# Kernel tuning notes

Measured on AMD Instinct MI355X. Metric: run time of the kernel, lower is better.

The kernel has to match this reference:

```python
import jax, jax.numpy as jnp
import numpy as np

B, T, C, H = 4, 4096, 1024, 64

def setup_inputs() -> dict:
    key = jax.random.key(0)
    k1, k2, k3, k4 = jax.random.split(key, 4)
    x = jax.random.normal(k1, (B, T, C), dtype=jnp.float32)
    # nn.Linear(C, H, bias=False): y = x @ W^T with W [H, C]; store as [C, H] for x @ W
    Wq = jax.random.normal(k2, (C, H), dtype=jnp.float32) * (C ** -0.5)
    Wk = jax.random.normal(k3, (C, H), dtype=jnp.float32) * (C ** -0.5)
    Wv = jax.random.normal(k4, (C, H), dtype=jnp.float32) * (C ** -0.5)
    return {"x": x, "Wq": Wq, "Wk": Wk, "Wv": Wv}

def reference(x, Wq, Wk, Wv):
    # Manual causal single-head attention (dropout p=0 -> identity).
    q = x @ Wq  # [B, T, H]
    k = x @ Wk  # [B, T, H]
    v = x @ Wv  # [B, T, H]
    scale = q.shape[-1] ** -0.5
    w = jnp.einsum('bth,bsh->bts', q, k) * scale  # [B, T, T] scores
    causal = jnp.tril(jnp.ones((x.shape[1], x.shape[1]), dtype=bool))
    w = jnp.where(causal, w, -jnp.inf)
    w = jax.nn.softmax(w, axis=-1)
    out = jnp.einsum('bts,bsh->bth', w, v)  # [B, T, H]
    return out
```

## Files before the change

kernel.cpp:

```cpp
#include <hip/hip_runtime.h>
#include <math.h>

#define Bn 4
#define Tn 4096
#define Cn 1024
#define Hn 64

typedef __attribute__((ext_vector_type(8))) short short8;
typedef __attribute__((ext_vector_type(4))) float floatx4;
typedef unsigned short ushort_t;

#define QSCALE 0.1803368801111204f

__device__ __forceinline__ ushort_t f2bf(float f) {
  union { float f; unsigned u; } v; v.f = f;
  unsigned r = v.u + 0x7FFFu + ((v.u >> 16) & 1u);
  return (ushort_t)(r >> 16);
}
__device__ __forceinline__ ushort_t f2bf_hu(float f) {
  union { float f; unsigned u; } v; v.f = f;
  return (ushort_t)((v.u + 0x8000u) >> 16);
}
__device__ __forceinline__ float bf2f(ushort_t h) {
  union { unsigned u; float f; } v; v.u = ((unsigned)h) << 16; return v.f;
}


__global__ __launch_bounds__(256) void wf_kernel(
    const float* __restrict__ Wq, const float* __restrict__ Wk,
    const float* __restrict__ Wv, ushort_t* __restrict__ Wf)
{
  __shared__ float ws[32][65];
  const int tid = threadIdx.x;
  const int m = blockIdx.x >> 5;
  const int g = blockIdx.x & 31;
  const float* W = (m == 0) ? Wq : (m == 1) ? Wk : Wv;
  const float4* src = (const float4*)(W + (size_t)g * 32 * Hn);
#pragma unroll
  for (int it = 0; it < 2; ++it) {
    int i4 = it * 256 + tid;
    float4 v = src[i4];
    int c = i4 >> 4, h = (i4 & 15) * 4;
    ws[c][h] = v.x; ws[c][h + 1] = v.y; ws[c][h + 2] = v.z; ws[c][h + 3] = v.w;
  }
  __syncthreads();
  const int nt = tid >> 6, lane = tid & 63;
  const int col = lane & 15, quad = lane >> 4;
  ushort_t t[8];
#pragma unroll
  for (int e = 0; e < 8; ++e) t[e] = f2bf(ws[quad * 8 + e][nt * 16 + col]);
  *(short8*)(Wf + ((size_t)((m * 32 + g) * 4 + nt) * 64 + lane) * 8) = *(short8*)t;
}

__global__ __launch_bounds__(256, 2) void qkv_proj_kernel(
    const float* __restrict__ x, const ushort_t* __restrict__ Wf,
    ushort_t* __restrict__ Qf, ushort_t* __restrict__ Kf,
    ushort_t* __restrict__ Vf)
{
  __shared__ __align__(16) char smem[49152];
  ushort_t* red = (ushort_t*)smem;
  ushort_t* img = (ushort_t*)smem;

  const int tid  = threadIdx.x;
  const int wv   = tid >> 6;
  const int lane = tid & 63;
  const int col  = lane & 15;
  const int quad = lane >> 4;
  const int blk  = blockIdx.x;
  const int row0 = blk * 32;

  floatx4 acc[2][3][4];
#pragma unroll
  for (int sub = 0; sub < 2; ++sub)
#pragma unroll
    for (int m = 0; m < 3; ++m)
#pragma unroll
      for (int nt = 0; nt < 4; ++nt) {
        acc[sub][m][nt][0] = 0.f; acc[sub][m][nt][1] = 0.f;
        acc[sub][m][nt][2] = 0.f; acc[sub][m][nt][3] = 0.f;
      }

#pragma unroll
  for (int ch = 0; ch < 8; ++ch) {
    const int gg = wv * 8 + ch;
    short8 af[2];
#pragma unroll
    for (int sub = 0; sub < 2; ++sub) {
      const float* xp = x + (size_t)(row0 + sub * 16 + col) * Cn + gg * 32 + quad * 8;
      float4 a0 = *(const float4*)(xp);
      float4 a1 = *(const float4*)(xp + 4);
      ushort_t t[8];
      t[0] = f2bf(a0.x); t[1] = f2bf(a0.y); t[2] = f2bf(a0.z); t[3] = f2bf(a0.w);
      t[4] = f2bf(a1.x); t[5] = f2bf(a1.y); t[6] = f2bf(a1.z); t[7] = f2bf(a1.w);
      af[sub] = *(short8*)t;
    }
#pragma unroll
    for (int m = 0; m < 3; ++m)
#pragma unroll
      for (int nt = 0; nt < 4; ++nt) {
        short8 bf = *(const short8*)(Wf + ((size_t)((m * 32 + gg) * 4 + nt) * 64 + lane) * 8);
        acc[0][m][nt] = __builtin_amdgcn_mfma_f32_16x16x32_bf16(af[0], bf, acc[0][m][nt], 0, 0, 0);
        acc[1][m][nt] = __builtin_amdgcn_mfma_f32_16x16x32_bf16(af[1], bf, acc[1][m][nt], 0, 0, 0);
      }
  }

#pragma unroll
  for (int sub = 0; sub < 2; ++sub)
#pragma unroll
    for (int m = 0; m < 3; ++m)
#pragma unroll
      for (int nt = 0; nt < 4; ++nt) {
        const int p = (sub * 3 + m) * 4 + nt;
        ushort4 u;
        u.x = f2bf(acc[sub][m][nt][0]); u.y = f2bf(acc[sub][m][nt][1]);
        u.z = f2bf(acc[sub][m][nt][2]); u.w = f2bf(acc[sub][m][nt][3]);
        *(ushort4*)&red[((p * 4 + wv) * 64 + lane) * 4] = u;
      }
  __syncthreads();

  float v[6][4];
#pragma unroll
  for (int pp = 0; pp < 6; ++pp) {
    const int p = wv * 6 + pp;
    ushort4 w0 = *(const ushort4*)&red[((p * 4 + 0) * 64 + lane) * 4];
    ushort4 w1 = *(const ushort4*)&red[((p * 4 + 1) * 64 + lane) * 4];
    ushort4 w2 = *(const ushort4*)&red[((p * 4 + 2) * 64 + lane) * 4];
    ushort4 w3 = *(const ushort4*)&red[((p * 4 + 3) * 64 + lane) * 4];
    v[pp][0] = (bf2f(w0.x) + bf2f(w1.x)) + (bf2f(w2.x) + bf2f(w3.x));
    v[pp][1] = (bf2f(w0.y) + bf2f(w1.y)) + (bf2f(w2.y) + bf2f(w3.y));
    v[pp][2] = (bf2f(w0.z) + bf2f(w1.z)) + (bf2f(w2.z) + bf2f(w3.z));
    v[pp][3] = (bf2f(w0.w) + bf2f(w1.w)) + (bf2f(w2.w) + bf2f(w3.w));
  }
  __syncthreads();

#pragma unroll
  for (int pp = 0; pp < 6; ++pp) {
    const int p = wv * 6 + pp;
    const int sub = (p >= 12) ? 1 : 0;
    const int mrem = p - sub * 12;
    const int m = mrem >> 2, nt = mrem & 3;
#pragma unroll
    for (int r = 0; r < 4; ++r) {
      const int tlq = quad * 4 + r;
      if (m == 2) {
        img[4096 + nt * 512 + (tlq >> 2) * 128 + col * 8 + (tlq & 3) * 2 + sub] = f2bf(v[pp][r]);
      } else {
        const int h = nt * 16 + col;
        const int idx = (h >> 5) * 512 + ((h >> 3) & 3) * 128 + tlq * 8 + (h & 7);
        img[m * 2048 + sub * 1024 + idx] = f2bf(m == 0 ? v[pp][r] * QSCALE : v[pp][r]);
      }
    }
  }
  __syncthreads();

  {
    const int b = blk >> 7, g = blk & 127;
#pragma unroll
    for (int sub = 0; sub < 2; ++sub) {
      const size_t qg = (size_t)(b * 256 + 2 * g + sub) * 1024 + tid * 4;
      *(uint2*)(Qf + qg) = *(const uint2*)&img[sub * 1024 + tid * 4];
      *(uint2*)(Kf + qg) = *(const uint2*)&img[2048 + sub * 1024 + tid * 4];
    }
    const int ht = tid >> 6;
    const size_t vg = ((size_t)(b * 64 + (g >> 1)) * 8 + ht * 2 + (g & 1)) * 512 + (tid & 63) * 8;
    *(short8*)(Vf + vg) = *(const short8*)&img[4096 + ht * 512 + (tid & 63) * 8];
  }
}

__global__ __launch_bounds__(256, 2) void attn_kernel(
    const ushort_t* __restrict__ Qf, const ushort_t* __restrict__ Kf,
    const ushort_t* __restrict__ Vf, float* __restrict__ out)
{
  __shared__ __align__(16) ushort_t Ps[4][2][16][72];
  __shared__ __align__(16) float Om[4][2][16][68];
  __shared__ __align__(16) float Ml[4][2][16];

  const int tid  = threadIdx.x;
  const int wv   = tid >> 6;
  const int lane = tid & 63;
  const int col  = lane & 15;
  const int quad = lane >> 4;
  const int b = blockIdx.x & 3;
  const int g = 127 - (blockIdx.x >> 2);

  short8 qf[2][2];
#pragma unroll
  for (int sub = 0; sub < 2; ++sub)
#pragma unroll
    for (int half = 0; half < 2; ++half)
      qf[sub][half] = *(const short8*)(Qf + (size_t)(b * 256 + 2 * g + sub) * 1024 + half * 512 + lane * 8);

  const ushort_t* Kbase = Kf + (size_t)b * 256 * 1024;
  const ushort_t* Vbase = Vf + (size_t)b * 64 * 8 * 512;

  short8 ones;
#pragma unroll
  for (int e = 0; e < 8; ++e) ones[e] = (short)0x3F80;

  floatx4 o[2][4], ol[2];
#pragma unroll
  for (int sub = 0; sub < 2; ++sub) {
#pragma unroll
    for (int ht = 0; ht < 4; ++ht) { o[sub][ht][0]=0.f; o[sub][ht][1]=0.f; o[sub][ht][2]=0.f; o[sub][ht][3]=0.f; }
    ol[sub][0]=0.f; ol[sub][1]=0.f; ol[sub][2]=0.f; ol[sub][3]=0.f;
  }

  const int ntile = ((g * 32 + 31) >> 6) + 1;
  const int dtile = ntile - 1;

  short8 kf[8], kfn[8];
#pragma unroll
  for (int kt = 0; kt < 4; ++kt) {
    const ushort_t* kp = Kbase + (size_t)wv * 4096 + kt * 1024 + lane * 8;
    kf[kt * 2]     = *(const short8*)(kp);
    kf[kt * 2 + 1] = *(const short8*)(kp + 512);
  }

  for (int i = wv; i < ntile; i += 4) {
    short8 vf[8];
#pragma unroll
    for (int ht = 0; ht < 4; ++ht) {
#pragma unroll
      for (int kh = 0; kh < 2; ++kh)
        vf[ht * 2 + kh] = *(const short8*)(Vbase + ((size_t)i * 8 + ht * 2 + kh) * 512 + lane * 8);
    }
#pragma unroll
    for (int kt = 0; kt < 4; ++kt) {
      const ushort_t* kp = Kbase + (size_t)(i + 4) * 4096 + kt * 1024 + lane * 8;
      kfn[kt * 2]     = *(const short8*)(kp);
      kfn[kt * 2 + 1] = *(const short8*)(kp + 512);
    }

    floatx4 s[2][4];
#pragma unroll
    for (int sub = 0; sub < 2; ++sub)
#pragma unroll
      for (int kt = 0; kt < 4; ++kt) {
        floatx4 c; c[0]=0.f; c[1]=0.f; c[2]=0.f; c[3]=0.f;
        c = __builtin_amdgcn_mfma_f32_16x16x32_bf16(qf[sub][0], kf[kt * 2],     c, 0, 0, 0);
        c = __builtin_amdgcn_mfma_f32_16x16x32_bf16(qf[sub][1], kf[kt * 2 + 1], c, 0, 0, 0);
        s[sub][kt] = c;
      }

    if (i == dtile) {
#pragma unroll
      for (int sub = 0; sub < 2; ++sub)
#pragma unroll
        for (int kt = 0; kt < 4; ++kt)
#pragma unroll
          for (int r = 0; r < 4; ++r)
            if (64 * i + kt * 16 + col > g * 32 + sub * 16 + quad * 4 + r)
              s[sub][kt][r] = -INFINITY;
    }

#pragma unroll
    for (int sub = 0; sub < 2; ++sub)
#pragma unroll
      for (int kt = 0; kt < 4; ++kt)
#pragma unroll
        for (int r = 0; r < 4; ++r)
          s[sub][kt][r] = __builtin_amdgcn_exp2f(s[sub][kt][r]);

#pragma unroll
    for (int sub = 0; sub < 2; ++sub)
#pragma unroll
      for (int r = 0; r < 4; ++r)
#pragma unroll
        for (int kh = 0; kh < 2; ++kh) {
          unsigned lo = f2bf_hu(s[sub][kh * 2][r]);
          unsigned hi = f2bf_hu(s[sub][kh * 2 + 1][r]);
          *(unsigned*)&Ps[wv][sub][quad * 4 + r][kh * 32 + col * 2] = (hi << 16) | lo;
        }

    short8 pf[2][2];
#pragma unroll
    for (int sub = 0; sub < 2; ++sub) {
      pf[sub][0] = *(const short8*)&Ps[wv][sub][col][quad * 8];
      pf[sub][1] = *(const short8*)&Ps[wv][sub][col][32 + quad * 8];
    }

#pragma unroll
    for (int sub = 0; sub < 2; ++sub) {
#pragma unroll
      for (int ht = 0; ht < 4; ++ht) {
        o[sub][ht] = __builtin_amdgcn_mfma_f32_16x16x32_bf16(pf[sub][0], vf[ht * 2],     o[sub][ht], 0, 0, 0);
        o[sub][ht] = __builtin_amdgcn_mfma_f32_16x16x32_bf16(pf[sub][1], vf[ht * 2 + 1], o[sub][ht], 0, 0, 0);
      }
      ol[sub] = __builtin_amdgcn_mfma_f32_16x16x32_bf16(pf[sub][0], ones, ol[sub], 0, 0, 0);
      ol[sub] = __builtin_amdgcn_mfma_f32_16x16x32_bf16(pf[sub][1], ones, ol[sub], 0, 0, 0);
    }

#pragma unroll
    for (int u2 = 0; u2 < 8; ++u2) kf[u2] = kfn[u2];
  }

#pragma unroll
  for (int sub = 0; sub < 2; ++sub) {
#pragma unroll
    for (int ht = 0; ht < 4; ++ht)
#pragma unroll
      for (int r = 0; r < 4; ++r)
        Om[wv][sub][quad * 4 + r][ht * 16 + col] = o[sub][ht][r];
    if (col == 0) {
#pragma unroll
      for (int r = 0; r < 4; ++r) Ml[wv][sub][quad * 4 + r] = ol[sub][r];
    }
  }
  __syncthreads();

  const int rr = tid >> 4, h4 = (tid & 15) * 4;
#pragma unroll
  for (int sub = 0; sub < 2; ++sub) {
    float L = (Ml[0][sub][rr] + Ml[1][sub][rr]) + (Ml[2][sub][rr] + Ml[3][sub][rr]);
    float4 a; a.x = 0.f; a.y = 0.f; a.z = 0.f; a.w = 0.f;
#pragma unroll
    for (int w = 0; w < 4; ++w) {
      float4 ov = *(const float4*)&Om[w][sub][rr][h4];
      a.x += ov.x; a.y += ov.y; a.z += ov.z; a.w += ov.w;
    }
    float inv = 1.f / L;
    a.x *= inv; a.y *= inv; a.z *= inv; a.w *= inv;
    *(float4*)(out + (size_t)(b * Tn + g * 32 + sub * 16 + rr) * Hn + h4) = a;
  }
}

extern "C" void kernel_launch(void* const* d_in, const int* in_sizes, int n_in,
                              void* d_out, int out_size, void* d_ws, size_t ws_size,
                              hipStream_t stream) {
  const float* x  = (const float*)d_in[0];
  const float* Wq = (const float*)d_in[1];
  const float* Wk = (const float*)d_in[2];
  const float* Wv = (const float*)d_in[3];
  float* out = (float*)d_out;

  ushort_t* Qf = (ushort_t*)d_ws;
  ushort_t* Kf = Qf + (size_t)Bn * Tn * Hn;
  ushort_t* Vf = Kf + (size_t)Bn * Tn * Hn;
  ushort_t* Wf = Vf + (size_t)Bn * Tn * Hn;

  wf_kernel<<<dim3(96), dim3(256), 0, stream>>>(Wq, Wk, Wv, Wf);
  qkv_proj_kernel<<<dim3(512), dim3(256), 0, stream>>>(x, Wf, Qf, Kf, Vf);
  attn_kernel<<<dim3(Bn * 128), dim3(256), 0, stream>>>(Qf, Kf, Vf, out);
}
```

Before: 134.2 us.

## Stage x tile through LDS in projection and interleave attention block order

The projection kernel now loads each wave's 32x256 x slice with coalesced float4 reads, converts it to bf16 into a padded LDS buffer, and then feeds the MFMA A fragments from LDS. This replaces the scattered per-lane global reads. The output image moves to a separate LDS region, which removes one barrier and lets the reduction write directly. LDS use grows to 66KB, which may limit how many blocks fit per CU. The attention kernel reorders its causal query blocks so odd heavy tiles are dispatched first and even light tiles last, aiming to balance load across CUs.

After: 125.6 us. 1.07x faster.

```diff
diff --git a/kernel.cpp b/kernel.cpp
--- a/kernel.cpp
+++ b/kernel.cpp
@@ -57,9 +57,10 @@
     ushort_t* __restrict__ Qf, ushort_t* __restrict__ Kf,
     ushort_t* __restrict__ Vf)
 {
-  __shared__ __align__(16) char smem[49152];
+  __shared__ __align__(16) char smem[67584];
+  ushort_t* xs  = (ushort_t*)smem;
   ushort_t* red = (ushort_t*)smem;
-  ushort_t* img = (ushort_t*)smem;
+  ushort_t* img = (ushort_t*)(smem + 49152);
 
   const int tid  = threadIdx.x;
   const int wv   = tid >> 6;
@@ -69,6 +70,14 @@
   const int blk  = blockIdx.x;
   const int row0 = blk * 32;
 
+#pragma unroll
+  for (int jj = 0; jj < 32; ++jj) {
+    float4 v = *(const float4*)(x + (size_t)(row0 + jj) * Cn + wv * 256 + lane * 4);
+    ushort4 u;
+    u.x = f2bf(v.x); u.y = f2bf(v.y); u.z = f2bf(v.z); u.w = f2bf(v.w);
+    *(ushort4*)(xs + (wv * 32 + jj) * 264 + lane * 4) = u;
+  }
+
   floatx4 acc[2][3][4];
 #pragma unroll
   for (int sub = 0; sub < 2; ++sub)
@@ -85,15 +94,8 @@
     const int gg = wv * 8 + ch;
     short8 af[2];
 #pragma unroll
-    for (int sub = 0; sub < 2; ++sub) {
-      const float* xp = x + (size_t)(row0 + sub * 16 + col) * Cn + gg * 32 + quad * 8;
-      float4 a0 = *(const float4*)(xp);
-      float4 a1 = *(const float4*)(xp + 4);
-      ushort_t t[8];
-      t[0] = f2bf(a0.x); t[1] = f2bf(a0.y); t[2] = f2bf(a0.z); t[3] = f2bf(a0.w);
-      t[4] = f2bf(a1.x); t[5] = f2bf(a1.y); t[6] = f2bf(a1.z); t[7] = f2bf(a1.w);
-      af[sub] = *(short8*)t;
-    }
+    for (int sub = 0; sub < 2; ++sub)
+      af[sub] = *(const short8*)(xs + (wv * 32 + sub * 16 + col) * 264 + ch * 32 + quad * 8);
 #pragma unroll
     for (int m = 0; m < 3; ++m)
 #pragma unroll
@@ -103,6 +105,7 @@
         acc[1][m][nt] = __builtin_amdgcn_mfma_f32_16x16x32_bf16(af[1], bf, acc[1][m][nt], 0, 0, 0);
       }
   }
+  __syncthreads();
 
 #pragma unroll
   for (int sub = 0; sub < 2; ++sub)
@@ -118,7 +121,6 @@
       }
   __syncthreads();
 
-  float v[6][4];
 #pragma unroll
   for (int pp = 0; pp < 6; ++pp) {
     const int p = wv * 6 + pp;
@@ -126,16 +128,11 @@
     ushort4 w1 = *(const ushort4*)&red[((p * 4 + 1) * 64 + lane) * 4];
     ushort4 w2 = *(const ushort4*)&red[((p * 4 + 2) * 64 + lane) * 4];
     ushort4 w3 = *(const ushort4*)&red[((p * 4 + 3) * 64 + lane) * 4];
-    v[pp][0] = (bf2f(w0.x) + bf2f(w1.x)) + (bf2f(w2.x) + bf2f(w3.x));
-    v[pp][1] = (bf2f(w0.y) + bf2f(w1.y)) + (bf2f(w2.y) + bf2f(w3.y));
-    v[pp][2] = (bf2f(w0.z) + bf2f(w1.z)) + (bf2f(w2.z) + bf2f(w3.z));
-    v[pp][3] = (bf2f(w0.w) + bf2f(w1.w)) + (bf2f(w2.w) + bf2f(w3.w));
-  }
-  __syncthreads();
-
-#pragma unroll
-  for (int pp = 0; pp < 6; ++pp) {
-    const int p = wv * 6 + pp;
+    float v[4];
+    v[0] = (bf2f(w0.x) + bf2f(w1.x)) + (bf2f(w2.x) + bf2f(w3.x));
+    v[1] = (bf2f(w0.y) + bf2f(w1.y)) + (bf2f(w2.y) + bf2f(w3.y));
+    v[2] = (bf2f(w0.z) + bf2f(w1.z)) + (bf2f(w2.z) + bf2f(w3.z));
+    v[3] = (bf2f(w0.w) + bf2f(w1.w)) + (bf2f(w2.w) + bf2f(w3.w));
     const int sub = (p >= 12) ? 1 : 0;
     const int mrem = p - sub * 12;
     const int m = mrem >> 2, nt = mrem & 3;
@@ -143,11 +140,11 @@
     for (int r = 0; r < 4; ++r) {
       const int tlq = quad * 4 + r;
       if (m == 2) {
-        img[4096 + nt * 512 + (tlq >> 2) * 128 + col * 8 + (tlq & 3) * 2 + sub] = f2bf(v[pp][r]);
+        img[4096 + nt * 512 + (tlq >> 2) * 128 + col * 8 + (tlq & 3) * 2 + sub] = f2bf(v[r]);
       } else {
         const int h = nt * 16 + col;
         const int idx = (h >> 5) * 512 + ((h >> 3) & 3) * 128 + tlq * 8 + (h & 7);
-        img[m * 2048 + sub * 1024 + idx] = f2bf(m == 0 ? v[pp][r] * QSCALE : v[pp][r]);
+        img[m * 2048 + sub * 1024 + idx] = f2bf(m == 0 ? v[r] * QSCALE : v[r]);
       }
     }
   }
@@ -180,8 +177,9 @@
   const int lane = tid & 63;
   const int col  = lane & 15;
   const int quad = lane >> 4;
-  const int b = blockIdx.x & 3;
-  const int g = 127 - (blockIdx.x >> 2);
+  const int b   = blockIdx.x & 3;
+  const int idx = blockIdx.x >> 2;
+  const int g   = (idx < 64) ? (127 - 2 * idx) : (2 * (idx - 64));
 
   short8 qf[2][2];
 #pragma unroll
```
